# Kernel optimization log

Hardware: AMD Instinct MI355X
Metric: run time of the kernel (lower is better)

## Reference

```python
import jax, jax.numpy as jnp
import numpy as np

N_QUBITS = 6
N_SHARED_LAYERS = 3
N_TASK_LAYERS = 2
ENC_HIDDEN = 256
INPUT_DIM = 784
BATCH = 256
P1Q = 0.001  # 1-qubit depolarizing prob
P2Q = 0.01   # 2-qubit-gate depolarizing approximation (applied as 1q channel, as in source)

C = jnp.complex64
PX = jnp.array([[0, 1], [1, 0]], C)
PY = jnp.array([[0, -1j], [1j, 0]], C)
PZ = jnp.array([[1, 0], [0, -1]], C)
CNOT = jnp.array([[1, 0, 0, 0], [0, 1, 0, 0], [0, 0, 0, 1], [0, 0, 1, 0]], C)

_LOW = 'abcdefghijklmnopqrstuvwxyz'


def _apply(dm, G, axes, batched):
    # contract gate G (rows=out, cols=in) into dm along absolute dm axes `axes`
    k = len(axes)
    G = G.reshape(G.shape[:G.ndim - 2] + (2,) * (2 * k))
    nd = dm.ndim - 1  # 2 * n_qubits
    dm_sub = ['Z'] + list(_LOW[:nd])
    out_sub = list(dm_sub)
    new = 'ABCD'
    gout, gin = [], []
    for j, ax in enumerate(axes):
        gout.append(new[j]); gin.append(dm_sub[ax]); out_sub[ax] = new[j]
    g_str = ('Z' if batched else '') + ''.join(gout) + ''.join(gin)
    return jnp.einsum(f"{g_str},{''.join(dm_sub)}->{''.join(out_sub)}", G, dm)


def apply_unitary(dm, U, wires, n, batched=False):
    # rho -> U rho U^dagger; ket axes are 1+w, bra axes 1+n+w
    dm = _apply(dm, U, [1 + w for w in wires], batched)
    return _apply(dm, jnp.conj(U), [1 + n + w for w in wires], batched)


def depolarize(dm, p, q, n):
    x = apply_unitary(dm, PX, [q], n)
    y = apply_unitary(dm, PY, [q], n)
    z = apply_unitary(dm, PZ, [q], n)
    return (1.0 - p) * dm + (p / 3.0) * (x + y + z)


def rot_mat(phi, theta, omega):
    # PennyLane Rot(phi, theta, omega) = RZ(omega) RY(theta) RZ(phi)
    c = jnp.cos(theta / 2)
    s = jnp.sin(theta / 2)
    ep = jnp.exp(-0.5j * (phi + omega))  # e^{-i(phi+omega)/2}
    em = jnp.exp(0.5j * (phi - omega))   # e^{+i(phi-omega)/2}
    return jnp.stack([jnp.stack([ep * c, -em * s]),
                      jnp.stack([jnp.conj(em) * s, jnp.conj(ep) * c])]).astype(C)


def ry_batched(theta):
    # theta: (B,) -> (B,2,2)
    c = jnp.cos(theta / 2)
    s = jnp.sin(theta / 2)
    return jnp.stack([jnp.stack([c, -s], -1),
                      jnp.stack([s, c], -1)], -2).astype(C)


def strongly_entangling(dm, w, n):
    # PennyLane StronglyEntanglingLayers, default ranges r = (l % (n-1)) + 1, CNOT ring
    L = w.shape[0]
    for l in range(L):
        for i in range(n):
            dm = apply_unitary(dm, rot_mat(w[l, i, 0], w[l, i, 1], w[l, i, 2]), [i], n)
        r = (l % (n - 1)) + 1
        for i in range(n):
            dm = apply_unitary(dm, CNOT, [i, (i + r) % n], n)
    return dm


def circuit(z, shared_w, task_w):
    n = N_QUBITS
    Bz = z.shape[0]
    dm = jnp.zeros((Bz,) + (2,) * (2 * n), C).at[(slice(None),) + (0,) * (2 * n)].set(1.0)
    for i in range(n):
        dm = apply_unitary(dm, ry_batched(z[:, i] * jnp.pi), [i], n, batched=True)
        dm = depolarize(dm, P1Q, i, n)
    dm = strongly_entangling(dm, shared_w, n)
    for i in range(n):
        dm = depolarize(dm, P1Q, i, n)
    for i in range(n - 1):
        dm = depolarize(dm, P2Q, i, n)
    dm = strongly_entangling(dm, task_w, n)
    for i in range(n):
        dm = depolarize(dm, P1Q, i, n)
    D = 2 ** n
    probs = jnp.real(jnp.diagonal(dm.reshape(Bz, D, D), axis1=1, axis2=2))  # (B, D)
    bits = (jnp.arange(D)[:, None] >> jnp.arange(n - 1, -1, -1)[None, :]) & 1  # wire 0 = MSB
    signs = (1 - 2 * bits).astype(jnp.float32)  # (D, n)
    return probs.astype(jnp.float32) @ signs    # (B, n) = <Z_i>


def setup_inputs():
    key = jax.random.key(0)
    ks = jax.random.split(key, 8)
    f = jnp.float32
    return {
        "x": jax.random.normal(ks[0], (BATCH, INPUT_DIM), f),
        "W1": jax.random.normal(ks[1], (ENC_HIDDEN, INPUT_DIM), f) * 0.03,
        "b1": jnp.zeros((ENC_HIDDEN,), f),
        "ln_g": jnp.ones((ENC_HIDDEN,), f),
        "ln_b": jnp.zeros((ENC_HIDDEN,), f),
        "W2": jax.random.normal(ks[2], (N_QUBITS, ENC_HIDDEN), f) * 0.05,
        "b2": jnp.zeros((N_QUBITS,), f),
        "shared_w": jax.random.normal(ks[3], (N_SHARED_LAYERS, N_QUBITS, 3), f) * 0.1,
        "task_w": jax.random.normal(ks[4], (N_TASK_LAYERS, N_QUBITS, 3), f) * 0.1,
        "Wp": jax.random.normal(ks[5], (2, N_QUBITS), f) * 0.1,
        "bp": jnp.zeros((2,), f),
    }


def reference(x, W1, b1, ln_g, ln_b, W2, b2, shared_w, task_w, Wp, bp):
    # encoder: Linear -> ReLU -> LayerNorm -> Linear -> Tanh
    h = jnp.maximum(x @ W1.T + b1, 0.0)
    mu = h.mean(-1, keepdims=True)
    var = ((h - mu) ** 2).mean(-1, keepdims=True)
    h = (h - mu) / jnp.sqrt(var + 1e-5) * ln_g + ln_b
    z = jnp.tanh(h @ W2.T + b2)            # (B, N_QUBITS)
    ev = circuit(z, shared_w, task_w)      # (B, N_QUBITS)
    return ev @ Wp.T + bp                  # (B, 2)
```

## Files before the change

kernel.cpp:

```cpp
#include <hip/hip_runtime.h>
#include <math.h>

#define NQ 6
#define BLK 1024
#define HID 256
#define INDIM 784

#define PW1 0.001f
#define PW2 0.01f
constexpr float WO1 = 1.f - 4.f * PW1 / 3.f;
constexpr float WO2 = 1.f - 4.f * PW2 / 3.f;
constexpr float WOc = WO1 * WO2;

struct alignas(16) RingTabs { int t[3][4096]; };
constexpr RingTabs make_ring_tabs() {
    RingTabs R{};
    for (int ri = 0; ri < 3; ++ri) {
        int r = ri + 1;
        for (int v = 0; v < 4096; ++v) {
            int x[6], z[6];
            for (int w = 0; w < 6; ++w) { x[w] = (v >> (2 * w + 1)) & 1; z[w] = (v >> (2 * w)) & 1; }
            int sgn = 0;
            for (int i = 5; i >= 0; --i) {
                int c = i, tg = (i + r) % 6;
                sgn ^= x[c] & z[tg] & (x[tg] ^ z[c] ^ 1);
                x[tg] ^= x[c];
                z[c]  ^= z[tg];
            }
            int s = 0;
            for (int w = 0; w < 6; ++w) s |= (x[w] << (2 * w + 1)) | (z[w] << (2 * w));
            R.t[ri][v] = s | (sgn << 31);
        }
    }
    return R;
}
static __device__ const RingTabs RT = make_ring_tabs();

__device__ __forceinline__ int swz(int n) {
    return n ^ ((((n >> 6) ^ (n >> 10)) & 3) << 3);
}

template<int CTRL>
__device__ __forceinline__ float qb(float v) {
    int r = __builtin_amdgcn_update_dpp(0, __builtin_bit_cast(int, v), CTRL, 0xF, 0xF, true);
    return __builtin_bit_cast(float, r);
}
template<int OFF>
__device__ __forceinline__ float swzl(float v) {
    return __builtin_bit_cast(float, __builtin_amdgcn_ds_swizzle(__builtin_bit_cast(int, v), OFF));
}

__device__ __forceinline__ void rot_reg(float e[4], float4 rZ, float4 rX, float4 rY) {
    float X = e[2], Y = e[3], Z = e[1];
    e[2] = fmaf(rX.x, X, fmaf(rX.y, Y, rX.z * Z));
    e[3] = fmaf(rY.x, X, fmaf(rY.y, Y, rY.z * Z));
    e[1] = fmaf(rZ.x, X, fmaf(rZ.y, Y, rZ.z * Z));
}
__device__ __forceinline__ void rot_q1(float e[4], float4 cf) {
    #pragma unroll
    for (int j = 0; j < 4; ++j) {
        float vZ = qb<0x55>(e[j]);
        float vX = qb<0xAA>(e[j]);
        float vY = qb<0xFF>(e[j]);
        e[j] = fmaf(cf.x, vX, fmaf(cf.y, vY, fmaf(cf.z, vZ, cf.w * e[j])));
    }
}
__device__ __forceinline__ void rot_q2(float e[4], float4 cf) {
    #pragma unroll
    for (int j = 0; j < 4; ++j) {
        float vZ = swzl<0x093>(e[j]);
        float vX = swzl<0x113>(e[j]);
        float vY = swzl<0x193>(e[j]);
        e[j] = fmaf(cf.x, vX, fmaf(cf.y, vY, fmaf(cf.z, vZ, cf.w * e[j])));
    }
}
__device__ __forceinline__ void rot_q3(float e[4], float4 cf, int lane) {
    int s1 = (lane & 15) | 16, s2 = (lane & 15) | 32, s3 = (lane & 15) | 48;
    #pragma unroll
    for (int j = 0; j < 4; ++j) {
        float vZ = __shfl(e[j], s1, 64);
        float vX = __shfl(e[j], s2, 64);
        float vY = __shfl(e[j], s3, 64);
        e[j] = fmaf(cf.x, vX, fmaf(cf.y, vY, fmaf(cf.z, vZ, cf.w * e[j])));
    }
}

__global__ __launch_bounds__(256)
void enc_gemm(const float* __restrict__ x, const float* __restrict__ W1,
              float* __restrict__ hp)
{
    __shared__ float xsT[196][32];
    __shared__ float wsT[196][32];
    const int tid = threadIdx.x;
    const int bid = blockIdx.x;
    const int tile = bid >> 2, s = bid & 3;
    const int bb = (tile >> 3) * 32, bu = (tile & 7) * 32;
    const int k0 = s * 196;

    for (int i = tid; i < 3136; i += 256) {
        int r = i & 31;
        int cb = i >> 5;
        int m = (cb >= 49);
        int c = cb - m * 49;
        const float* src = m ? (W1 + (size_t)(bu + r) * INDIM + k0 + 4 * c)
                             : (x  + (size_t)(bb + r) * INDIM + k0 + 4 * c);
        float4 v = *(const float4*)src;
        float (*dst)[32] = m ? wsT : xsT;
        dst[4 * c + 0][r] = v.x;
        dst[4 * c + 1][r] = v.y;
        dst[4 * c + 2][r] = v.z;
        dst[4 * c + 3][r] = v.w;
    }
    __syncthreads();

    const int tx = tid & 15, ty = tid >> 4;
    float a00 = 0.f, a01 = 0.f, a10 = 0.f, a11 = 0.f;
    #pragma unroll 4
    for (int k = 0; k < 196; ++k) {
        float2 xv = *(const float2*)&xsT[k][2 * ty];
        float2 wv = *(const float2*)&wsT[k][2 * tx];
        a00 = fmaf(xv.x, wv.x, a00);
        a01 = fmaf(xv.x, wv.y, a01);
        a10 = fmaf(xv.y, wv.x, a10);
        a11 = fmaf(xv.y, wv.y, a11);
    }
    float* o = hp + (size_t)s * 65536 + (size_t)(bb + 2 * ty) * 256 + bu + 2 * tx;
    o[0] = a00; o[1] = a01;
    o[256] = a10; o[257] = a11;
}

__global__ __launch_bounds__(BLK)
void nqm_kernel(const float* __restrict__ hp, const float* __restrict__ b1,
                const float* __restrict__ ln_g, const float* __restrict__ ln_b,
                const float* __restrict__ W2, const float* __restrict__ b2,
                const float* __restrict__ shared_w, const float* __restrict__ task_w,
                const float* __restrict__ Wp, const float* __restrict__ bp,
                float* __restrict__ out)
{
    __shared__ __align__(16) float dmA[4096];
    __shared__ __align__(16) float dmB[4096];
    __shared__ __align__(16) float4 Mlane[30][4];
    __shared__ float bloch[NQ][4];
    __shared__ float red[4], red2[4];
    __shared__ float zpart[4][8];
    __shared__ float bcast[2];
    __shared__ float evs[8];

    const int tid = threadIdx.x;
    const int b = blockIdx.x;
    const int wv = tid >> 6;
    const int lane = tid & 63;

    float h = 0.0f;
    if (tid < 256) {
        const float* hb = hp + (size_t)b * 256 + tid;
        h = hb[0] + hb[65536] + hb[131072] + hb[196608] + b1[tid];
        h = fmaxf(h, 0.0f);
        float s = h, s2 = h * h;
        #pragma unroll
        for (int off = 32; off > 0; off >>= 1) {
            s  += __shfl_down(s, off, 64);
            s2 += __shfl_down(s2, off, 64);
        }
        if (lane == 0) { red[tid >> 6] = s; red2[tid >> 6] = s2; }
    }
    __syncthreads();
    if (tid == 0) {
        float ts  = red[0] + red[1] + red[2] + red[3];
        float ts2 = red2[0] + red2[1] + red2[2] + red2[3];
        float mu  = ts * (1.0f / HID);
        float var = ts2 * (1.0f / HID) - mu * mu;
        bcast[0] = mu;
        bcast[1] = rsqrtf(var + 1e-5f);
    }
    __syncthreads();
    if (tid < 256) {
        float hnj = (h - bcast[0]) * bcast[1] * ln_g[tid] + ln_b[tid];
        float p[NQ];
        #pragma unroll
        for (int i = 0; i < NQ; ++i) p[i] = hnj * W2[i * HID + tid];
        #pragma unroll
        for (int off = 32; off > 0; off >>= 1) {
            #pragma unroll
            for (int i = 0; i < NQ; ++i) p[i] += __shfl_down(p[i], off, 64);
        }
        if (lane == 0) {
            #pragma unroll
            for (int i = 0; i < NQ; ++i) zpart[tid >> 6][i] = p[i];
        }
    }
    __syncthreads();

    if (tid < NQ) {
        float z = zpart[0][tid] + zpart[1][tid] + zpart[2][tid] + zpart[3][tid] + b2[tid];
        z = tanhf(z);
        float sn, c;
        sincosf(z * 3.14159265358979323846f, &sn, &c);
        bloch[tid][0] = 1.0f;
        bloch[tid][1] = WO1 * c;
        bloch[tid][2] = WO1 * sn;
        bloch[tid][3] = 0.0f;
    } else if (tid < 36) {
        int g = tid - NQ;
        int layer = g / NQ;
        int wire = g % NQ;
        const float* w = (layer < 3) ? (shared_w + (layer * NQ + wire) * 3)
                                     : (task_w + ((layer - 3) * NQ + wire) * 3);
        float phi = w[0], theta = w[1], omega = w[2];
        float sf, cf_, st, ct, so, co;
        sincosf(phi, &sf, &cf_);
        sincosf(theta, &st, &ct);
        sincosf(omega, &so, &co);
        float M00 = co * ct * cf_ - so * sf;
        float M01 = -co * ct * sf - so * cf_;
        float M02 = co * st;
        float M10 = so * ct * cf_ + co * sf;
        float M11 = -so * ct * sf + co * cf_;
        float M12 = so * st;
        float M20 = -st * cf_;
        float M21 = st * sf;
        float M22 = ct;
        float f = (layer == 3) ? ((wire < 5) ? WOc : WO1) : 1.0f;
        Mlane[g][0] = make_float4(0.f, 0.f, 0.f, 1.f);
        Mlane[g][1] = make_float4(f * M20, f * M21, f * M22, 0.f);
        Mlane[g][2] = make_float4(f * M00, f * M01, f * M02, 0.f);
        Mlane[g][3] = make_float4(f * M10, f * M11, f * M12, 0.f);
    }

    const int q1 = lane & 3, q2 = (lane >> 2) & 3, q3 = (lane >> 4) & 3;
    const int q4 = wv & 3, q5 = wv >> 2;
    const int baseB = ((lane & 3) << 10) | (wv << 4) | (lane >> 2);
    const int rtab[4] = {0, 1, 2, 0};
    __syncthreads();

    for (int l = 0; l < 5; ++l) {
        const int g0 = l * 6;
        float e[4];

        if (l == 0) {
            float A = bloch[1][q1] * bloch[2][q2] * bloch[3][q3] * bloch[4][q4] * bloch[5][q5];
            e[0] = A * bloch[0][0];
            e[1] = A * bloch[0][1];
            e[2] = A * bloch[0][2];
            e[3] = A * bloch[0][3];
        } else {
            const int4 te = *(const int4*)&RT.t[rtab[l - 1]][tid << 2];
            float v0 = dmA[swz(te.x & 4095)];
            float v1 = dmA[swz(te.y & 4095)];
            float v2 = dmA[swz(te.z & 4095)];
            float v3 = dmA[swz(te.w & 4095)];
            e[0] = __int_as_float(__float_as_int(v0) ^ (te.x & 0x80000000));
            e[1] = __int_as_float(__float_as_int(v1) ^ (te.y & 0x80000000));
            e[2] = __int_as_float(__float_as_int(v2) ^ (te.z & 0x80000000));
            e[3] = __int_as_float(__float_as_int(v3) ^ (te.w & 0x80000000));
        }
        rot_reg(e, Mlane[g0 + 0][1], Mlane[g0 + 0][2], Mlane[g0 + 0][3]);
        rot_q1(e, Mlane[g0 + 1][q1]);
        rot_q2(e, Mlane[g0 + 2][q2]);
        rot_q3(e, Mlane[g0 + 3][q3], lane);
        *(float4*)&dmB[swz(tid << 2)] = make_float4(e[0], e[1], e[2], e[3]);
        __syncthreads();

        e[0] = dmB[swz(baseB)];
        e[1] = dmB[swz(baseB + 256)];
        e[2] = dmB[swz(baseB + 512)];
        e[3] = dmB[swz(baseB + 768)];
        rot_reg(e, Mlane[g0 + 4][1], Mlane[g0 + 4][2], Mlane[g0 + 4][3]);
        rot_q1(e, Mlane[g0 + 5][lane & 3]);
        dmA[swz(baseB)]       = e[0];
        dmA[swz(baseB + 256)] = e[1];
        dmA[swz(baseB + 512)] = e[2];
        dmA[swz(baseB + 768)] = e[3];
        __syncthreads();
    }

    if (tid < NQ) {
        int e = RT.t[1][1 << (2 * tid)];
        float v = dmA[swz(e & 4095)];
        v = __int_as_float(__float_as_int(v) ^ (e & 0x80000000));
        evs[tid] = WO1 * v;
    }
    __syncthreads();
    if (tid < 2) {
        float o = bp[tid];
        #pragma unroll
        for (int i = 0; i < NQ; ++i) o = fmaf(evs[i], Wp[tid * NQ + i], o);
        out[b * 2 + tid] = o;
    }
}

extern "C" void kernel_launch(void* const* d_in, const int* in_sizes, int n_in,
                              void* d_out, int out_size, void* d_ws, size_t ws_size,
                              hipStream_t stream) {
    (void)in_sizes; (void)n_in; (void)ws_size; (void)out_size;
    const float* x        = (const float*)d_in[0];
    const float* W1       = (const float*)d_in[1];
    const float* b1       = (const float*)d_in[2];
    const float* ln_g     = (const float*)d_in[3];
    const float* ln_b     = (const float*)d_in[4];
    const float* W2       = (const float*)d_in[5];
    const float* b2       = (const float*)d_in[6];
    const float* shared_w = (const float*)d_in[7];
    const float* task_w   = (const float*)d_in[8];
    const float* Wp       = (const float*)d_in[9];
    const float* bp       = (const float*)d_in[10];
    float* out = (float*)d_out;
    float* hp  = (float*)d_ws;

    hipLaunchKernelGGL(enc_gemm, dim3(256), dim3(256), 0, stream, x, W1, hp);
    hipLaunchKernelGGL(nqm_kernel, dim3(256), dim3(BLK), 0, stream,
                       hp, b1, ln_g, ln_b, W2, b2, shared_w, task_w, Wp, bp, out);
}
```

Before: 95.53 us.

## Retile encoder GEMM to 64x64 tiles with 4x4 register blocking and 14-way split-K

The encoder GEMM moves from 32x32 output tiles with 2x2 per-thread accumulators and 4-way split-K to 64x64 tiles with 4x4 per-thread accumulators and 14-way split-K, keeping roughly the same block count (224). This raises arithmetic intensity per shared-memory load, uses float4 LDS reads and stores, and cuts shared memory per block. In exchange the partial-sum workspace grows to 14 slices, so the downstream kernel now reads and sums 14 partials per hidden element instead of 4, adding global memory traffic.

Measured after the change: 95.25 us. Within noise of the previous version (-0.3%).

```diff
diff --git a/kernel.cpp b/kernel.cpp
--- a/kernel.cpp
+++ b/kernel.cpp
@@ -5,6 +5,8 @@
 #define BLK 1024
 #define HID 256
 #define INDIM 784
+#define KC 56
+#define NSPLIT 14
 
 #define PW1 0.001f
 #define PW2 0.01f
@@ -89,23 +91,25 @@
 void enc_gemm(const float* __restrict__ x, const float* __restrict__ W1,
               float* __restrict__ hp)
 {
-    __shared__ float xsT[196][32];
-    __shared__ float wsT[196][32];
+    __shared__ float xsT[KC][64];
+    __shared__ float wsT[KC][64];
     const int tid = threadIdx.x;
     const int bid = blockIdx.x;
-    const int tile = bid >> 2, s = bid & 3;
-    const int bb = (tile >> 3) * 32, bu = (tile & 7) * 32;
-    const int k0 = s * 196;
-
-    for (int i = tid; i < 3136; i += 256) {
-        int r = i & 31;
-        int cb = i >> 5;
-        int m = (cb >= 49);
-        int c = cb - m * 49;
+    const int tile = bid / NSPLIT;
+    const int s = bid - tile * NSPLIT;
+    const int bb = (tile >> 2) * 64;
+    const int bu = (tile & 3) * 64;
+    const int k0 = s * KC;
+
+    for (int i = tid; i < 1792; i += 256) {
+        int r = i & 63;
+        int cb = i >> 6;
+        int m = (cb >= 14);
+        int c = cb - m * 14;
         const float* src = m ? (W1 + (size_t)(bu + r) * INDIM + k0 + 4 * c)
                              : (x  + (size_t)(bb + r) * INDIM + k0 + 4 * c);
         float4 v = *(const float4*)src;
-        float (*dst)[32] = m ? wsT : xsT;
+        float (*dst)[64] = m ? wsT : xsT;
         dst[4 * c + 0][r] = v.x;
         dst[4 * c + 1][r] = v.y;
         dst[4 * c + 2][r] = v.z;
@@ -114,19 +118,23 @@
     __syncthreads();
 
     const int tx = tid & 15, ty = tid >> 4;
-    float a00 = 0.f, a01 = 0.f, a10 = 0.f, a11 = 0.f;
-    #pragma unroll 4
-    for (int k = 0; k < 196; ++k) {
-        float2 xv = *(const float2*)&xsT[k][2 * ty];
-        float2 wv = *(const float2*)&wsT[k][2 * tx];
-        a00 = fmaf(xv.x, wv.x, a00);
-        a01 = fmaf(xv.x, wv.y, a01);
-        a10 = fmaf(xv.y, wv.x, a10);
-        a11 = fmaf(xv.y, wv.y, a11);
-    }
-    float* o = hp + (size_t)s * 65536 + (size_t)(bb + 2 * ty) * 256 + bu + 2 * tx;
-    o[0] = a00; o[1] = a01;
-    o[256] = a10; o[257] = a11;
+    float acc[4][4] = {};
+    #pragma unroll 7
+    for (int k = 0; k < KC; ++k) {
+        float4 xv = *(const float4*)&xsT[k][4 * ty];
+        float4 wv = *(const float4*)&wsT[k][4 * tx];
+        const float xa[4] = {xv.x, xv.y, xv.z, xv.w};
+        const float wa[4] = {wv.x, wv.y, wv.z, wv.w};
+        #pragma unroll
+        for (int i = 0; i < 4; ++i)
+            #pragma unroll
+            for (int j = 0; j < 4; ++j)
+                acc[i][j] = fmaf(xa[i], wa[j], acc[i][j]);
+    }
+    float* o = hp + (size_t)s * 65536 + (size_t)(bb + 4 * ty) * 256 + bu + 4 * tx;
+    #pragma unroll
+    for (int i = 0; i < 4; ++i)
+        *(float4*)(o + (size_t)i * 256) = make_float4(acc[i][0], acc[i][1], acc[i][2], acc[i][3]);
 }
 
 __global__ __launch_bounds__(BLK)
@@ -154,7 +162,9 @@
     float h = 0.0f;
     if (tid < 256) {
         const float* hb = hp + (size_t)b * 256 + tid;
-        h = hb[0] + hb[65536] + hb[131072] + hb[196608] + b1[tid];
+        h = b1[tid];
+        #pragma unroll
+        for (int s = 0; s < NSPLIT; ++s) h += hb[(size_t)s * 65536];
         h = fmaxf(h, 0.0f);
         float s = h, s2 = h * h;
         #pragma unroll
@@ -307,7 +317,7 @@
     float* out = (float*)d_out;
     float* hp  = (float*)d_ws;
 
-    hipLaunchKernelGGL(enc_gemm, dim3(256), dim3(256), 0, stream, x, W1, hp);
+    hipLaunchKernelGGL(enc_gemm, dim3(16 * NSPLIT), dim3(256), 0, stream, x, W1, hp);
     hipLaunchKernelGGL(nqm_kernel, dim3(256), dim3(BLK), 0, stream,
                        hp, b1, ln_g, ln_b, W2, b2, shared_w, task_w, Wp, bp, out);
 }
```
